# Kernel tuning notes

Hardware: AMD Instinct MI355X
Metric: run time of the kernel (lower is better)

The kernel has to match this reference:

```python
import jax, jax.numpy as jnp
import numpy as np

B, T, D = 8, 2048, 1024
FF = 4 * D
EPS = 1e-5


def setup_inputs() -> dict:
    key = jax.random.key(0)
    ks = jax.random.split(key, 20)
    rn = lambda k, s, sc=0.02: (jax.random.normal(k, s, jnp.float32) * sc)
    return {
        "x": jax.random.normal(ks[0], (B, T, D), jnp.float32),
        "ln1_g": jnp.ones((D,), jnp.float32),
        "ln1_b": jnp.zeros((D,), jnp.float32),
        "ln2_g": jnp.ones((D,), jnp.float32),
        "ln2_b": jnp.zeros((D,), jnp.float32),
        # time-mixing lerp coefficients in [0,1]
        "tm_mix_k": jax.random.uniform(ks[1], (D,), jnp.float32),
        "tm_mix_v": jax.random.uniform(ks[2], (D,), jnp.float32),
        "tm_mix_r": jax.random.uniform(ks[3], (D,), jnp.float32),
        # per-channel decay (log-log space, w = -exp(time_decay)) and first-token bonus
        "time_decay": rn(ks[4], (D,), 1.0),
        "time_first": rn(ks[5], (D,), 0.5),
        "wk": rn(ks[6], (D, D)),
        "wv": rn(ks[7], (D, D)),
        "wr": rn(ks[8], (D, D)),
        "wo": rn(ks[9], (D, D)),
        "cm_mix_k": jax.random.uniform(ks[10], (D,), jnp.float32),
        "cm_mix_r": jax.random.uniform(ks[11], (D,), jnp.float32),
        "cwk": rn(ks[12], (D, FF)),
        "cwv": rn(ks[13], (FF, D)),
        "cwr": rn(ks[14], (D, D)),
    }


def layer_norm(x, g, b):
    mu = jnp.mean(x, axis=-1, keepdims=True)
    var = jnp.var(x, axis=-1, keepdims=True)
    return (x - mu) * jax.lax.rsqrt(var + EPS) * g + b


def token_shift(x):
    # x[:, t-1] with zeros at t=0 (fresh state)
    return jnp.pad(x, ((0, 0), (1, 0), (0, 0)))[:, :-1]


def wkv_scan(k, v, time_decay, time_first):
    """Numerically-stable RWKV-4 WKV linear recurrence. k,v: [B,T,D]."""
    w = -jnp.exp(time_decay)  # [D], negative log-decay per step
    u = time_first

    def step(carry, kv):
        aa, bb, pp = carry  # each [B, D]
        kt, vt = kv
        ww = u + kt
        p = jnp.maximum(pp, ww)
        e1 = jnp.exp(pp - p)
        e2 = jnp.exp(ww - p)
        out = (e1 * aa + e2 * vt) / (e1 * bb + e2)
        ww2 = pp + w
        p2 = jnp.maximum(ww2, kt)
        e1b = jnp.exp(ww2 - p2)
        e2b = jnp.exp(kt - p2)
        return (e1b * aa + e2b * vt, e1b * bb + e2b, p2), out

    z = jnp.zeros((k.shape[0], k.shape[2]), k.dtype)
    init = (z, z, jnp.full_like(z, -1e38))
    _, outs = jax.lax.scan(step, init, (jnp.moveaxis(k, 1, 0), jnp.moveaxis(v, 1, 0)))
    return jnp.moveaxis(outs, 0, 1)  # [B,T,D]


def reference(x, ln1_g, ln1_b, ln2_g, ln2_b,
              tm_mix_k, tm_mix_v, tm_mix_r, time_decay, time_first,
              wk, wv, wr, wo, cm_mix_k, cm_mix_r, cwk, cwv, cwr):
    # --- Time mixing (pre-LN residual) ---
    h = layer_norm(x, ln1_g, ln1_b)
    hx = token_shift(h)
    k = jnp.einsum("btd,de->bte", h * tm_mix_k + hx * (1.0 - tm_mix_k), wk)
    v = jnp.einsum("btd,de->bte", h * tm_mix_v + hx * (1.0 - tm_mix_v), wv)
    r = jax.nn.sigmoid(jnp.einsum("btd,de->bte", h * tm_mix_r + hx * (1.0 - tm_mix_r), wr))
    wkv = wkv_scan(k, v, time_decay, time_first)
    x = x + jnp.einsum("btd,de->bte", r * wkv, wo)

    # --- Channel mixing (pre-LN residual) ---
    h = layer_norm(x, ln2_g, ln2_b)
    hx = token_shift(h)
    kk = jnp.einsum("btd,df->btf", h * cm_mix_k + hx * (1.0 - cm_mix_k), cwk)
    kk = jnp.square(jax.nn.relu(kk))  # [B,T,4D]
    rr = jax.nn.sigmoid(jnp.einsum("btd,de->bte", h * cm_mix_r + hx * (1.0 - cm_mix_r), cwr))
    x = x + rr * jnp.einsum("btf,fd->btd", kk, cwv)
    return x
```

## Files before the change

### kernel.cpp

```cpp
#include <hip/hip_runtime.h>

typedef unsigned short u16;
typedef float f32x4 __attribute__((ext_vector_type(4)));
typedef __bf16 bf16x8 __attribute__((ext_vector_type(8)));
typedef u16 u16x8 __attribute__((ext_vector_type(8)));
typedef u16 u16x4 __attribute__((ext_vector_type(4)));

static constexpr int D  = 1024;
static constexpr int T  = 2048;
static constexpr int NB = 8;
static constexpr int M  = NB * T;
static constexpr int FF = 4096;
static constexpr int NCH = 32;
static constexpr int CL  = T / NCH;

__device__ __forceinline__ u16 f2bf(float f) {
  unsigned u = __builtin_bit_cast(unsigned, f);
  return (u16)((u + 0x7fffu + ((u >> 16) & 1u)) >> 16);
}
__device__ __forceinline__ float bf2f(u16 s) {
  return __builtin_bit_cast(float, (unsigned)s << 16);
}

__device__ __forceinline__ void gload16(const u16* g, u16* l) {
  __builtin_amdgcn_global_load_lds(
      (const __attribute__((address_space(1))) void*)g,
      (__attribute__((address_space(3))) void*)l, 16, 0, 0);
}

__global__ __launch_bounds__(256) void lnmix3_kernel(const float* __restrict__ x,
    const float* __restrict__ g, const float* __restrict__ b,
    const float* __restrict__ mk, const float* __restrict__ mv, const float* __restrict__ mr,
    u16* __restrict__ xk, u16* __restrict__ xv, u16* __restrict__ xr) {
  __shared__ float red[16];
  const int m = blockIdx.x, tid = threadIdx.x;
  const bool first = (m % T) == 0;
  f32x4 v = *(const f32x4*)&x[(size_t)m * D + tid * 4];
  f32x4 vp = {0.0f, 0.0f, 0.0f, 0.0f};
  if (!first) vp = *(const f32x4*)&x[(size_t)(m - 1) * D + tid * 4];
  float s  = v[0] + v[1] + v[2] + v[3];
  float s2 = v[0]*v[0] + v[1]*v[1] + v[2]*v[2] + v[3]*v[3];
  float p  = vp[0] + vp[1] + vp[2] + vp[3];
  float p2 = vp[0]*vp[0] + vp[1]*vp[1] + vp[2]*vp[2] + vp[3]*vp[3];
  #pragma unroll
  for (int o = 32; o > 0; o >>= 1) {
    s += __shfl_down(s, o); s2 += __shfl_down(s2, o);
    p += __shfl_down(p, o); p2 += __shfl_down(p2, o);
  }
  if ((tid & 63) == 0) {
    red[tid >> 6] = s; red[4 + (tid >> 6)] = s2;
    red[8 + (tid >> 6)] = p; red[12 + (tid >> 6)] = p2;
  }
  __syncthreads();
  s  = red[0] + red[1] + red[2] + red[3];
  s2 = red[4] + red[5] + red[6] + red[7];
  p  = red[8] + red[9] + red[10] + red[11];
  p2 = red[12] + red[13] + red[14] + red[15];
  const float mu  = s * (1.0f / D);
  const float rs  = rsqrtf(s2 * (1.0f / D) - mu * mu + 1e-5f);
  const float mup = p * (1.0f / D);
  const float rsp = rsqrtf(p2 * (1.0f / D) - mup * mup + 1e-5f);
  u16x4 ok, ov, orr;
  #pragma unroll
  for (int i = 0; i < 4; ++i) {
    const int d = tid * 4 + i;
    const float h  = (v[i] - mu) * rs * g[d] + b[d];
    const float hp = first ? 0.0f : (vp[i] - mup) * rsp * g[d] + b[d];
    float a;
    a = mk[d]; ok[i]  = f2bf(h * a + hp * (1.0f - a));
    a = mv[d]; ov[i]  = f2bf(h * a + hp * (1.0f - a));
    a = mr[d]; orr[i] = f2bf(h * a + hp * (1.0f - a));
  }
  const size_t base = (size_t)m * D + tid * 4;
  *(u16x4*)&xk[base] = ok;
  *(u16x4*)&xv[base] = ov;
  *(u16x4*)&xr[base] = orr;
}

__global__ __launch_bounds__(256) void lnmix2_kernel(const float* __restrict__ x,
    const float* __restrict__ g, const float* __restrict__ b,
    const float* __restrict__ mk, const float* __restrict__ mr,
    u16* __restrict__ xk, u16* __restrict__ xr) {
  __shared__ float red[16];
  const int m = blockIdx.x, tid = threadIdx.x;
  const bool first = (m % T) == 0;
  f32x4 v = *(const f32x4*)&x[(size_t)m * D + tid * 4];
  f32x4 vp = {0.0f, 0.0f, 0.0f, 0.0f};
  if (!first) vp = *(const f32x4*)&x[(size_t)(m - 1) * D + tid * 4];
  float s  = v[0] + v[1] + v[2] + v[3];
  float s2 = v[0]*v[0] + v[1]*v[1] + v[2]*v[2] + v[3]*v[3];
  float p  = vp[0] + vp[1] + vp[2] + vp[3];
  float p2 = vp[0]*vp[0] + vp[1]*vp[1] + vp[2]*vp[2] + vp[3]*vp[3];
  #pragma unroll
  for (int o = 32; o > 0; o >>= 1) {
    s += __shfl_down(s, o); s2 += __shfl_down(s2, o);
    p += __shfl_down(p, o); p2 += __shfl_down(p2, o);
  }
  if ((tid & 63) == 0) {
    red[tid >> 6] = s; red[4 + (tid >> 6)] = s2;
    red[8 + (tid >> 6)] = p; red[12 + (tid >> 6)] = p2;
  }
  __syncthreads();
  s  = red[0] + red[1] + red[2] + red[3];
  s2 = red[4] + red[5] + red[6] + red[7];
  p  = red[8] + red[9] + red[10] + red[11];
  p2 = red[12] + red[13] + red[14] + red[15];
  const float mu  = s * (1.0f / D);
  const float rs  = rsqrtf(s2 * (1.0f / D) - mu * mu + 1e-5f);
  const float mup = p * (1.0f / D);
  const float rsp = rsqrtf(p2 * (1.0f / D) - mup * mup + 1e-5f);
  u16x4 ok, orr;
  #pragma unroll
  for (int i = 0; i < 4; ++i) {
    const int d = tid * 4 + i;
    const float h  = (v[i] - mu) * rs * g[d] + b[d];
    const float hp = first ? 0.0f : (vp[i] - mup) * rsp * g[d] + b[d];
    float a;
    a = mk[d]; ok[i]  = f2bf(h * a + hp * (1.0f - a));
    a = mr[d]; orr[i] = f2bf(h * a + hp * (1.0f - a));
  }
  const size_t base = (size_t)m * D + tid * 4;
  *(u16x4*)&xk[base] = ok;
  *(u16x4*)&xr[base] = orr;
}

__global__ __launch_bounds__(256) void transpose_bf16_kernel(const float* __restrict__ in,
                                                             u16* __restrict__ out,
                                                             int K_, int N_) {
  __shared__ u16 t[32][33];
  const int k0 = blockIdx.x * 32, n0 = blockIdx.y * 32;
  const int r = threadIdx.x >> 5, c = threadIdx.x & 31;
  #pragma unroll
  for (int p = 0; p < 4; ++p)
    t[r + p * 8][c] = f2bf(in[(size_t)(k0 + r + p * 8) * N_ + n0 + c]);
  __syncthreads();
  #pragma unroll
  for (int p = 0; p < 4; ++p)
    out[(size_t)(n0 + r + p * 8) * K_ + k0 + c] = t[c][r + p * 8];
}

__global__ __launch_bounds__(256) void wkv_phase1(const u16* __restrict__ K_,
                                                  const u16* __restrict__ V_,
                                                  const float* __restrict__ td,
                                                  float* __restrict__ aggA,
                                                  float* __restrict__ aggB,
                                                  float* __restrict__ aggP) {
  const int gid = blockIdx.x * 256 + threadIdx.x;
  const int d = gid & (D - 1);
  const int c = (gid >> 10) & (NCH - 1);
  const int b = gid >> 15;
  const float w = -expf(td[d]);
  float a = 0.0f, bb = 0.0f, p = -1e38f;
  size_t idx = ((size_t)b * T + (size_t)c * CL) * D + d;
  for (int t = 0; t < CL; ++t, idx += D) {
    const float kt = bf2f(K_[idx]);
    const float vt = bf2f(V_[idx]);
    const float wp = p + w;
    const float pn = fmaxf(wp, kt);
    const float e1 = expf(wp - pn), e2 = expf(kt - pn);
    a  = e1 * a  + e2 * vt;
    bb = e1 * bb + e2;
    p  = pn;
  }
  aggA[gid] = a; aggB[gid] = bb; aggP[gid] = p;
}

__global__ __launch_bounds__(256) void wkv_phase2(const float* __restrict__ td,
                                                  const float* __restrict__ aggA,
                                                  const float* __restrict__ aggB,
                                                  const float* __restrict__ aggP,
                                                  float* __restrict__ incA,
                                                  float* __restrict__ incB,
                                                  float* __restrict__ incP) {
  const int gid = blockIdx.x * 256 + threadIdx.x;
  const int d = gid & (D - 1);
  const int b = gid >> 10;
  const float cw = -expf(td[d]) * (float)CL;
  float a = 0.0f, bb = 0.0f, p = -1e38f;
  for (int c = 0; c < NCH; ++c) {
    const int i = (b * NCH + c) * D + d;
    incA[i] = a; incB[i] = bb; incP[i] = p;
    const float pd = p + cw;
    const float pc = aggP[i];
    const float pn = fmaxf(pd, pc);
    const float e1 = expf(pd - pn), e2 = expf(pc - pn);
    a  = e1 * a  + e2 * aggA[i];
    bb = e1 * bb + e2 * aggB[i];
    p  = pn;
  }
}

__global__ __launch_bounds__(256) void wkv_phase3(const u16* __restrict__ K_,
                                                  const u16* __restrict__ V_,
                                                  const u16* __restrict__ R_,
                                                  const float* __restrict__ td,
                                                  const float* __restrict__ tf,
                                                  const float* __restrict__ incA,
                                                  const float* __restrict__ incB,
                                                  const float* __restrict__ incP,
                                                  u16* __restrict__ a2) {
  const int gid = blockIdx.x * 256 + threadIdx.x;
  const int d = gid & (D - 1);
  const int c = (gid >> 10) & (NCH - 1);
  const int b = gid >> 15;
  const float w = -expf(td[d]);
  const float u = tf[d];
  float aa = incA[gid], bb = incB[gid], pp = incP[gid];
  size_t idx = ((size_t)b * T + (size_t)c * CL) * D + d;
  for (int t = 0; t < CL; ++t, idx += D) {
    const float kt = bf2f(K_[idx]);
    const float vt = bf2f(V_[idx]);
    const float rt = bf2f(R_[idx]);
    const float ww = u + kt;
    const float p  = fmaxf(pp, ww);
    const float e1 = expf(pp - p), e2 = expf(ww - p);
    const float o  = (e1 * aa + e2 * vt) / (e1 * bb + e2);
    a2[idx] = f2bf(rt * o);
    const float ww2 = pp + w;
    const float p2  = fmaxf(ww2, kt);
    const float e1b = expf(ww2 - p2), e2b = expf(kt - p2);
    aa = e1b * aa + e2b * vt;
    bb = e1b * bb + e2b;
    pp = p2;
  }
}

template <int EPI>
__global__ __launch_bounds__(512, 2) void gemm8(const u16* __restrict__ A,
                                                const u16* __restrict__ Bt,
                                                int N, int K,
                                                float* __restrict__ outf,
                                                u16* __restrict__ outh,
                                                const float* __restrict__ auxf,
                                                const u16* __restrict__ auxh,
                                                float* __restrict__ dst) {
  __shared__ u16 sm[65536];
  const int gx = gridDim.x, gy = gridDim.y;
  const int fid = blockIdx.y * gx + blockIdx.x;
  const int xcd = fid & 7, sl = fid >> 3;
  const int m0 = (xcd * (gx >> 3) + sl / gy) * 256;
  const int n0 = (sl % gy) * 256;

  const int tid = threadIdx.x;
  const int w = tid >> 6, l = tid & 63;
  const int wm = w >> 2, wn = w & 3;
  const int lr = l >> 3, ls = l & 7;
  const int NT = K >> 6;
  f32x4 acc[8][4] = {};

  const u16* gA = A + (size_t)(m0 + w * 8 + lr) * K + (ls ^ lr) * 8;
  const u16* gB = Bt + (size_t)(n0 + w * 8 + lr) * K + (ls ^ lr) * 8;

  auto stA = [&](int j, int r) {
    gload16(gA + ((size_t)r * 64) * K + (size_t)j * 64,
            &sm[(j & 1) * 16384 + (r * 64 + w * 8) * 64]);
  };
  auto stB = [&](int j, int r) {
    gload16(gB + ((size_t)r * 64) * K + (size_t)j * 64,
            &sm[32768 + (j & 1) * 16384 + (r * 64 + w * 8) * 64]);
  };

  u16x8 bF[4][2], aF[2][2];

  auto ldB8 = [&](const u16* sB) {
    #pragma unroll
    for (int ni = 0; ni < 4; ++ni)
      #pragma unroll
      for (int ks = 0; ks < 2; ++ks) {
        const int rb = wn * 64 + ni * 16 + (l & 15);
        const int rs = ks * 4 + (l >> 4);
        bF[ni][ks] = *(const u16x8*)&sB[rb * 64 + ((rs ^ (rb & 7)) * 8)];
      }
  };

#define LDA(q, sAp)                                                         \
  _Pragma("unroll") for (int mi = 0; mi < 2; ++mi)                          \
    _Pragma("unroll") for (int ks = 0; ks < 2; ++ks) {                      \
      const int ra = wm * 128 + (q) * 32 + mi * 16 + (l & 15);              \
      const int rs = ks * 4 + (l >> 4);                                     \
      aF[mi][ks] = *(const u16x8*)&sAp[ra * 64 + ((rs ^ (ra & 7)) * 8)];    \
    }

#define MFMA16(Q)                                                           \
  __builtin_amdgcn_s_setprio(1);                                            \
  _Pragma("unroll") for (int ks = 0; ks < 2; ++ks)                          \
    _Pragma("unroll") for (int mi = 0; mi < 2; ++mi)                        \
      _Pragma("unroll") for (int ni = 0; ni < 4; ++ni)                      \
        acc[(Q) * 2 + mi][ni] = __builtin_amdgcn_mfma_f32_16x16x32_bf16(    \
            __builtin_bit_cast(bf16x8, aF[mi][ks]),                         \
            __builtin_bit_cast(bf16x8, bF[ni][ks]),                         \
            acc[(Q) * 2 + mi][ni], 0, 0, 0);                                \
  __builtin_amdgcn_s_setprio(0);

#define LGKM0_FENCE                                                         \
  asm volatile("s_waitcnt lgkmcnt(0)" ::: "memory");                        \
  __builtin_amdgcn_sched_barrier(0);

  stB(0, 0); stB(0, 1); stB(0, 2); stB(0, 3);
  stA(0, 0); stA(0, 1); stA(0, 2); stA(0, 3);
  if (1 < NT) {
    stB(1, 0); stB(1, 1); stB(1, 2); stB(1, 3);
    stA(1, 0); stA(1, 1); stA(1, 2); stA(1, 3);
    asm volatile("s_waitcnt vmcnt(8)" ::: "memory");
  } else {
    asm volatile("s_waitcnt vmcnt(0)" ::: "memory");
  }
  __builtin_amdgcn_s_barrier();

  for (int k = 0; k < NT; ++k) {
    const u16* sA = &sm[(k & 1) * 16384];
    const u16* sB = &sm[32768 + (k & 1) * 16384];
    const bool s2 = (k + 2 < NT);
    ldB8(sB);
    LDA(0, sA);
    asm volatile("s_waitcnt lgkmcnt(8)" ::: "memory");
    __builtin_amdgcn_s_barrier();
    LGKM0_FENCE
    MFMA16(0);
    __builtin_amdgcn_s_barrier();
    LDA(1, sA);
    if (s2) { stB(k + 2, 0); stB(k + 2, 1); }
    __builtin_amdgcn_s_barrier();
    LGKM0_FENCE
    MFMA16(1);
    __builtin_amdgcn_s_barrier();
    LDA(2, sA);
    if (s2) { stB(k + 2, 2); stB(k + 2, 3); stA(k + 2, 0); stA(k + 2, 2); }
    __builtin_amdgcn_s_barrier();
    LGKM0_FENCE
    MFMA16(2);
    __builtin_amdgcn_s_barrier();
    LDA(3, sA);
    __builtin_amdgcn_s_barrier();
    LGKM0_FENCE
    if (s2) {
      stA(k + 2, 1); stA(k + 2, 3);
      asm volatile("s_waitcnt vmcnt(6)" ::: "memory");
    } else if (k + 1 < NT) {
      asm volatile("s_waitcnt vmcnt(0)" ::: "memory");
    }
    MFMA16(3);
    __builtin_amdgcn_s_barrier();
  }
#undef LDA
#undef MFMA16
#undef LGKM0_FENCE

  const int cl = l & 15, rh = l >> 4;
  #pragma unroll
  for (int mi = 0; mi < 8; ++mi) {
    #pragma unroll
    for (int ni = 0; ni < 4; ++ni) {
      const int gn = n0 + wn * 64 + ni * 16 + cl;
      #pragma unroll
      for (int j = 0; j < 4; ++j) {
        const int gm = m0 + wm * 128 + mi * 16 + rh * 4 + j;
        const float c = acc[mi][ni][j];
        const size_t o = (size_t)gm * N + gn;
        if (EPI == 0) outf[o] = c;
        else if (EPI == 1) outh[o] = f2bf(1.0f / (1.0f + expf(-c)));
        else if (EPI == 2) outf[o] = auxf[o] + c;
        else if (EPI == 3) { const float t = c > 0.0f ? c : 0.0f; outh[o] = f2bf(t * t); }
        else if (EPI == 4) dst[o] += bf2f(auxh[o]) * c;
        else if (EPI == 5) outh[o] = f2bf(c);
      }
    }
  }
}

extern "C" void kernel_launch(void* const* d_in, const int* in_sizes, int n_in,
                              void* d_out, int out_size, void* d_ws, size_t ws_size,
                              hipStream_t stream) {
  (void)in_sizes; (void)n_in; (void)out_size;
  const float* x      = (const float*)d_in[0];
  const float* ln1_g  = (const float*)d_in[1];
  const float* ln1_b  = (const float*)d_in[2];
  const float* ln2_g  = (const float*)d_in[3];
  const float* ln2_b  = (const float*)d_in[4];
  const float* tm_k   = (const float*)d_in[5];
  const float* tm_v   = (const float*)d_in[6];
  const float* tm_r   = (const float*)d_in[7];
  const float* tdec   = (const float*)d_in[8];
  const float* tfir   = (const float*)d_in[9];
  const float* wk     = (const float*)d_in[10];
  const float* wv     = (const float*)d_in[11];
  const float* wr     = (const float*)d_in[12];
  const float* wo     = (const float*)d_in[13];
  const float* cm_k   = (const float*)d_in[14];
  const float* cm_r   = (const float*)d_in[15];
  const float* cwk    = (const float*)d_in[16];
  const float* cwv    = (const float*)d_in[17];
  const float* cwr    = (const float*)d_in[18];
  float* out = (float*)d_out;

  const size_t MB = 1024 * 1024;
  if (ws_size < 218 * MB) return;

  char* w = (char*)d_ws;
  u16*   h    = (u16*)(w);
  u16*   b32  = (u16*)(w + 32 * MB);
  u16*   b64  = (u16*)(w + 64 * MB);
  u16*   b96  = (u16*)(w + 96 * MB);
  u16*   Kb   = (u16*)(w + 128 * MB);
  u16*   KK   = (u16*)(w + 64 * MB);
  u16*   wkT  = (u16*)(w + 192 * MB);
  u16*   wvT  = (u16*)(w + 194 * MB);
  u16*   wrT  = (u16*)(w + 196 * MB);
  u16*   woT  = (u16*)(w + 198 * MB);
  u16*   cwkT = (u16*)(w + 200 * MB);
  u16*   cwvT = (u16*)(w + 208 * MB);
  u16*   cwrT = (u16*)(w + 216 * MB);
  float* aggA = (float*)(w + 96 * MB);
  float* aggB = (float*)(w + 97 * MB);
  float* aggP = (float*)(w + 98 * MB);
  float* incA = (float*)(w + 99 * MB);
  float* incB = (float*)(w + 100 * MB);
  float* incP = (float*)(w + 101 * MB);

  transpose_bf16_kernel<<<dim3(D / 32, D / 32), 256, 0, stream>>>(wk, wkT, D, D);
  transpose_bf16_kernel<<<dim3(D / 32, D / 32), 256, 0, stream>>>(wv, wvT, D, D);
  transpose_bf16_kernel<<<dim3(D / 32, D / 32), 256, 0, stream>>>(wr, wrT, D, D);
  transpose_bf16_kernel<<<dim3(D / 32, D / 32), 256, 0, stream>>>(wo, woT, D, D);
  transpose_bf16_kernel<<<dim3(D / 32, FF / 32), 256, 0, stream>>>(cwk, cwkT, D, FF);
  transpose_bf16_kernel<<<dim3(FF / 32, D / 32), 256, 0, stream>>>(cwv, cwvT, FF, D);
  transpose_bf16_kernel<<<dim3(D / 32, D / 32), 256, 0, stream>>>(cwr, cwrT, D, D);

  lnmix3_kernel<<<M, 256, 0, stream>>>(x, ln1_g, ln1_b, tm_k, tm_v, tm_r, b32, b64, b96);

  dim3 gD(M / 256, D / 256);
  gemm8<5><<<gD, 512, 0, stream>>>(b32, wkT, D, D, nullptr, Kb, nullptr, nullptr, nullptr);
  gemm8<5><<<gD, 512, 0, stream>>>(b64, wvT, D, D, nullptr, b32, nullptr, nullptr, nullptr);
  gemm8<1><<<gD, 512, 0, stream>>>(b96, wrT, D, D, nullptr, h, nullptr, nullptr, nullptr);

  wkv_phase1<<<(NB * NCH * D) / 256, 256, 0, stream>>>(Kb, b32, tdec, aggA, aggB, aggP);
  wkv_phase2<<<(NB * D) / 256, 256, 0, stream>>>(tdec, aggA, aggB, aggP, incA, incB, incP);
  wkv_phase3<<<(NB * NCH * D) / 256, 256, 0, stream>>>(Kb, b32, h, tdec, tfir,
                                                       incA, incB, incP, b64);

  gemm8<2><<<gD, 512, 0, stream>>>(b64, woT, D, D, out, nullptr, x, nullptr, nullptr);

  lnmix2_kernel<<<M, 256, 0, stream>>>(out, ln2_g, ln2_b, cm_k, cm_r, b32, b64);

  gemm8<1><<<gD, 512, 0, stream>>>(b64, cwrT, D, D, nullptr, h, nullptr, nullptr, nullptr);

  dim3 gF(M / 256, FF / 256);
  gemm8<3><<<gF, 512, 0, stream>>>(b32, cwkT, FF, D, nullptr, KK, nullptr, nullptr, nullptr);

  dim3 gO(M / 256, D / 256);
  gemm8<4><<<gO, 512, 0, stream>>>(KK, cwvT, D, FF, nullptr, nullptr, nullptr, h, out);
}
```

Baseline: 710.8 us.

## Shrink GEMM tile to 256x128 with BK=32 and triple-buffered LDS

```diff
diff --git a/kernel.cpp b/kernel.cpp
--- a/kernel.cpp
+++ b/kernel.cpp
@@ -226,7 +226,7 @@
 }
 
 template <int EPI>
-__global__ __launch_bounds__(512, 2) void gemm8(const u16* __restrict__ A,
+__global__ __launch_bounds__(512, 4) void gemm8(const u16* __restrict__ A,
                                                 const u16* __restrict__ Bt,
                                                 int N, int K,
                                                 float* __restrict__ outf,
@@ -234,128 +234,107 @@
                                                 const float* __restrict__ auxf,
                                                 const u16* __restrict__ auxh,
                                                 float* __restrict__ dst) {
-  __shared__ u16 sm[65536];
+  __shared__ u16 sm[36864];
   const int gx = gridDim.x, gy = gridDim.y;
   const int fid = blockIdx.y * gx + blockIdx.x;
   const int xcd = fid & 7, sl = fid >> 3;
   const int m0 = (xcd * (gx >> 3) + sl / gy) * 256;
-  const int n0 = (sl % gy) * 256;
+  const int n0 = (sl % gy) * 128;
 
   const int tid = threadIdx.x;
   const int w = tid >> 6, l = tid & 63;
   const int wm = w >> 2, wn = w & 3;
-  const int lr = l >> 3, ls = l & 7;
-  const int NT = K >> 6;
-  f32x4 acc[8][4] = {};
-
-  const u16* gA = A + (size_t)(m0 + w * 8 + lr) * K + (ls ^ lr) * 8;
-  const u16* gB = Bt + (size_t)(n0 + w * 8 + lr) * K + (ls ^ lr) * 8;
+  const int NT = K >> 5;
+  f32x4 acc[8][2] = {};
+
+  const int srow = w * 16 + (l >> 2);
+  const int scol = 8 * ((l & 3) ^ ((l >> 3) & 3));
+  const u16* gA = A + (size_t)(m0 + srow) * K + scol;
+  const u16* gB = Bt + (size_t)(n0 + srow) * K + scol;
 
   auto stA = [&](int j, int r) {
-    gload16(gA + ((size_t)r * 64) * K + (size_t)j * 64,
-            &sm[(j & 1) * 16384 + (r * 64 + w * 8) * 64]);
+    gload16(gA + (size_t)r * 128 * K + (size_t)j * 32,
+            &sm[(j % 3) * 12288 + (r * 128 + w * 16) * 32]);
   };
-  auto stB = [&](int j, int r) {
-    gload16(gB + ((size_t)r * 64) * K + (size_t)j * 64,
-            &sm[32768 + (j & 1) * 16384 + (r * 64 + w * 8) * 64]);
+  auto stB = [&](int j) {
+    gload16(gB + (size_t)j * 32,
+            &sm[(j % 3) * 12288 + 8192 + (w * 16) * 32]);
   };
 
-  u16x8 bF[4][2], aF[2][2];
-
-  auto ldB8 = [&](const u16* sB) {
-    #pragma unroll
-    for (int ni = 0; ni < 4; ++ni)
-      #pragma unroll
-      for (int ks = 0; ks < 2; ++ks) {
-        const int rb = wn * 64 + ni * 16 + (l & 15);
-        const int rs = ks * 4 + (l >> 4);
-        bF[ni][ks] = *(const u16x8*)&sB[rb * 64 + ((rs ^ (rb & 7)) * 8)];
-      }
-  };
-
-#define LDA(q, sAp)                                                         \
-  _Pragma("unroll") for (int mi = 0; mi < 2; ++mi)                          \
-    _Pragma("unroll") for (int ks = 0; ks < 2; ++ks) {                      \
-      const int ra = wm * 128 + (q) * 32 + mi * 16 + (l & 15);              \
-      const int rs = ks * 4 + (l >> 4);                                     \
-      aF[mi][ks] = *(const u16x8*)&sAp[ra * 64 + ((rs ^ (ra & 7)) * 8)];    \
-    }
-
-#define MFMA16(Q)                                                           \
+  u16x8 aF[4], bF[2];
+
+#define LDB2(sBp)                                                           \
+  _Pragma("unroll") for (int ni = 0; ni < 2; ++ni) {                        \
+    const int rb = wn * 32 + ni * 16 + (l & 15);                            \
+    const int rs = (l >> 4) ^ ((rb >> 1) & 3);                              \
+    bF[ni] = *(const u16x8*)&sBp[rb * 32 + rs * 8];                         \
+  }
+
+#define LDA4(ph, sAp)                                                       \
+  _Pragma("unroll") for (int qi = 0; qi < 4; ++qi) {                        \
+    const int ra = wm * 128 + ((ph) * 4 + qi) * 16 + (l & 15);              \
+    const int rs = (l >> 4) ^ ((ra >> 1) & 3);                              \
+    aF[qi] = *(const u16x8*)&sAp[ra * 32 + rs * 8];                         \
+  }
+
+#define MFMA8(ph)                                                           \
   __builtin_amdgcn_s_setprio(1);                                            \
-  _Pragma("unroll") for (int ks = 0; ks < 2; ++ks)                          \
-    _Pragma("unroll") for (int mi = 0; mi < 2; ++mi)                        \
-      _Pragma("unroll") for (int ni = 0; ni < 4; ++ni)                      \
-        acc[(Q) * 2 + mi][ni] = __builtin_amdgcn_mfma_f32_16x16x32_bf16(    \
-            __builtin_bit_cast(bf16x8, aF[mi][ks]),                         \
-            __builtin_bit_cast(bf16x8, bF[ni][ks]),                         \
-            acc[(Q) * 2 + mi][ni], 0, 0, 0);                                \
+  _Pragma("unroll") for (int qi = 0; qi < 4; ++qi)                          \
+    _Pragma("unroll") for (int ni = 0; ni < 2; ++ni)                        \
+      acc[(ph) * 4 + qi][ni] = __builtin_amdgcn_mfma_f32_16x16x32_bf16(     \
+          __builtin_bit_cast(bf16x8, aF[qi]),                               \
+          __builtin_bit_cast(bf16x8, bF[ni]),                               \
+          acc[(ph) * 4 + qi][ni], 0, 0, 0);                                 \
   __builtin_amdgcn_s_setprio(0);
 
 #define LGKM0_FENCE                                                         \
   asm volatile("s_waitcnt lgkmcnt(0)" ::: "memory");                        \
   __builtin_amdgcn_sched_barrier(0);
 
-  stB(0, 0); stB(0, 1); stB(0, 2); stB(0, 3);
-  stA(0, 0); stA(0, 1); stA(0, 2); stA(0, 3);
+  stB(0); stA(0, 0); stA(0, 1);
   if (1 < NT) {
-    stB(1, 0); stB(1, 1); stB(1, 2); stB(1, 3);
-    stA(1, 0); stA(1, 1); stA(1, 2); stA(1, 3);
-    asm volatile("s_waitcnt vmcnt(8)" ::: "memory");
+    stB(1); stA(1, 0); stA(1, 1);
+    asm volatile("s_waitcnt vmcnt(3)" ::: "memory");
   } else {
     asm volatile("s_waitcnt vmcnt(0)" ::: "memory");
   }
   __builtin_amdgcn_s_barrier();
 
   for (int k = 0; k < NT; ++k) {
-    const u16* sA = &sm[(k & 1) * 16384];
-    const u16* sB = &sm[32768 + (k & 1) * 16384];
+    const u16* sA = &sm[(k % 3) * 12288];
+    const u16* sB = sA + 8192;
     const bool s2 = (k + 2 < NT);
-    ldB8(sB);
-    LDA(0, sA);
-    asm volatile("s_waitcnt lgkmcnt(8)" ::: "memory");
+    LDB2(sB);
+    LDA4(0, sA);
+    if (s2) { stB(k + 2); stA(k + 2, 0); }
     __builtin_amdgcn_s_barrier();
     LGKM0_FENCE
-    MFMA16(0);
+    MFMA8(0);
     __builtin_amdgcn_s_barrier();
-    LDA(1, sA);
-    if (s2) { stB(k + 2, 0); stB(k + 2, 1); }
+    LDA4(1, sA);
+    if (s2) stA(k + 2, 1);
     __builtin_amdgcn_s_barrier();
     LGKM0_FENCE
-    MFMA16(1);
+    MFMA8(1);
+    if (s2)      asm volatile("s_waitcnt vmcnt(3)" ::: "memory");
+    else if (k + 1 < NT) asm volatile("s_waitcnt vmcnt(0)" ::: "memory");
     __builtin_amdgcn_s_barrier();
-    LDA(2, sA);
-    if (s2) { stB(k + 2, 2); stB(k + 2, 3); stA(k + 2, 0); stA(k + 2, 2); }
-    __builtin_amdgcn_s_barrier();
-    LGKM0_FENCE
-    MFMA16(2);
-    __builtin_amdgcn_s_barrier();
-    LDA(3, sA);
-    __builtin_amdgcn_s_barrier();
-    LGKM0_FENCE
-    if (s2) {
-      stA(k + 2, 1); stA(k + 2, 3);
-      asm volatile("s_waitcnt vmcnt(6)" ::: "memory");
-    } else if (k + 1 < NT) {
-      asm volatile("s_waitcnt vmcnt(0)" ::: "memory");
-    }
-    MFMA16(3);
-    __builtin_amdgcn_s_barrier();
-  }
-#undef LDA
-#undef MFMA16
+  }
+#undef LDB2
+#undef LDA4
+#undef MFMA8
 #undef LGKM0_FENCE
 
   const int cl = l & 15, rh = l >> 4;
   #pragma unroll
-  for (int mi = 0; mi < 8; ++mi) {
+  for (int q = 0; q < 8; ++q) {
     #pragma unroll
-    for (int ni = 0; ni < 4; ++ni) {
-      const int gn = n0 + wn * 64 + ni * 16 + cl;
+    for (int ni = 0; ni < 2; ++ni) {
+      const int gn = n0 + wn * 32 + ni * 16 + cl;
       #pragma unroll
       for (int j = 0; j < 4; ++j) {
-        const int gm = m0 + wm * 128 + mi * 16 + rh * 4 + j;
-        const float c = acc[mi][ni][j];
+        const int gm = m0 + wm * 128 + q * 16 + rh * 4 + j;
+        const float c = acc[q][ni][j];
         const size_t o = (size_t)gm * N + gn;
         if (EPI == 0) outf[o] = c;
         else if (EPI == 1) outh[o] = f2bf(1.0f / (1.0f + expf(-c)));
@@ -427,7 +406,7 @@
 
   lnmix3_kernel<<<M, 256, 0, stream>>>(x, ln1_g, ln1_b, tm_k, tm_v, tm_r, b32, b64, b96);
 
-  dim3 gD(M / 256, D / 256);
+  dim3 gD(M / 256, D / 128);
   gemm8<5><<<gD, 512, 0, stream>>>(b32, wkT, D, D, nullptr, Kb, nullptr, nullptr, nullptr);
   gemm8<5><<<gD, 512, 0, stream>>>(b64, wvT, D, D, nullptr, b32, nullptr, nullptr, nullptr);
   gemm8<1><<<gD, 512, 0, stream>>>(b96, wrT, D, D, nullptr, h, nullptr, nullptr, nullptr);
@@ -443,9 +422,9 @@
 
   gemm8<1><<<gD, 512, 0, stream>>>(b64, cwrT, D, D, nullptr, h, nullptr, nullptr, nullptr);
 
-  dim3 gF(M / 256, FF / 256);
+  dim3 gF(M / 256, FF / 128);
   gemm8<3><<<gF, 512, 0, stream>>>(b32, cwkT, FF, D, nullptr, KK, nullptr, nullptr, nullptr);
 
-  dim3 gO(M / 256, D / 256);
+  dim3 gO(M / 256, D / 128);
   gemm8<4><<<gO, 512, 0, stream>>>(KK, cwvT, D, FF, nullptr, nullptr, nullptr, h, out);
 }
```

New measurement: 744.0 us. 4.7% more time.
